# Kernel tuning notes

Measured on AMD Instinct MI355X. Metric: run time of the kernel, lower is better.

Reference implementation:

```python
import jax, jax.numpy as jnp
import numpy as np

SCALE = 0.0078125  # dequant scale from init_kwargs


def setup_inputs() -> dict:
    key = jax.random.key(0)
    k1, k2, k3 = jax.random.split(key, 3)
    B, S, D_IN, D_OUT = 4, 2048, 2048, 8192
    x = jax.random.normal(k1, (B, S, D_IN), dtype=jnp.float32)
    weight = jax.random.normal(k2, (D_OUT, D_IN), dtype=jnp.float32)  # torch Linear layout
    bias = jax.random.normal(k3, (D_OUT,), dtype=jnp.float32)
    return {"x": x, "weight": weight, "bias": bias}


def reference(x, weight, bias):
    # MATMUL.apply(x, weight.t(), bias, scale): scaled matmul + fused bias
    # out[b,s,o] = scale * sum_i x[b,s,i] * weight[o,i] + bias[o]
    out = jnp.einsum('bsi,oi->bso', x, weight) * jnp.asarray(SCALE, x.dtype)
    return out + bias
```

## Files before the change

### kernel.cpp

```cpp
#include <hip/hip_runtime.h>
#include <hip/hip_bf16.h>
#include <stdint.h>

typedef __bf16 bf16x8 __attribute__((ext_vector_type(8)));
typedef float  f32x4  __attribute__((ext_vector_type(4)));

static constexpr float kScale = 0.0078125f;

static __device__ __forceinline__ uint32_t bf16_rne(float f) {
  uint32_t u = __builtin_bit_cast(uint32_t, f);
  u += 0x7FFFu + ((u >> 16) & 1u);
  return u >> 16;
}
static __device__ __forceinline__ uint32_t pack2(float lo, float hi) {
  return bf16_rne(lo) | (bf16_rne(hi) << 16);
}

__global__ __launch_bounds__(256) void cvt_f32_to_bf16(
    const float* __restrict__ src, uint4* __restrict__ dst) {
  const int i = blockIdx.x * 256 + threadIdx.x;
  const float4* sv = reinterpret_cast<const float4*>(src);
  float4 a = sv[2 * i];
  float4 b = sv[2 * i + 1];
  uint4 o;
  o.x = pack2(a.x, a.y);
  o.y = pack2(a.z, a.w);
  o.z = pack2(b.x, b.y);
  o.w = pack2(b.z, b.w);
  dst[i] = o;
}

static __device__ __forceinline__ void gload_lds16(const void* g, void* l) {
  __builtin_amdgcn_global_load_lds(
      (const __attribute__((address_space(1))) void*)g,
      (__attribute__((address_space(3))) void*)l, 16, 0, 0);
}

#define BARRIER() __builtin_amdgcn_s_barrier()
#define LGKM0()                                        \
  do {                                                 \
    asm volatile("s_waitcnt lgkmcnt(0)" ::: "memory"); \
    __builtin_amdgcn_sched_barrier(0);                 \
  } while (0)
#define LGKM8() asm volatile("s_waitcnt lgkmcnt(8)" ::: "memory")
#define VMW(n)                                               \
  do {                                                       \
    asm volatile("s_waitcnt vmcnt(" #n ")" ::: "memory");    \
    __builtin_amdgcn_sched_barrier(0);                       \
  } while (0)

constexpr int TILE_V = (256 * 64) / 8;

template <int MH, int NH>
__device__ __forceinline__ void quad(f32x4 (&acc)[8][4],
                                     const bf16x8 (&aF)[4][2],
                                     const bf16x8 (&bF)[2][2]) {
  __builtin_amdgcn_s_setprio(1);
#pragma unroll
  for (int mi = 0; mi < 4; ++mi)
#pragma unroll
    for (int ni = 0; ni < 2; ++ni)
#pragma unroll
      for (int kk = 0; kk < 2; ++kk)
        acc[MH * 4 + mi][NH * 2 + ni] = __builtin_amdgcn_mfma_f32_16x16x32_bf16(
            aF[mi][kk], bF[ni][kk], acc[MH * 4 + mi][NH * 2 + ni], 0, 0, 0);
  __builtin_amdgcn_s_setprio(0);
}

template <int BUF, int MH>
__device__ __forceinline__ void loadA(bf16x8 (&aF)[4][2], const bf16x8* Av,
                                      int wr, int fr, int ac0) {
#pragma unroll
  for (int mi = 0; mi < 4; ++mi) {
    const int row = (MH << 7) + (wr << 6) + (mi << 4) + fr;
    aF[mi][0] = Av[BUF * TILE_V + row * 8 + ac0];
    aF[mi][1] = Av[BUF * TILE_V + row * 8 + (ac0 ^ 4)];
  }
}
template <int BUF, int NH>
__device__ __forceinline__ void loadB(bf16x8 (&bF)[2][2], const bf16x8* Bv,
                                      int wc, int fr, int ac0) {
#pragma unroll
  for (int ni = 0; ni < 2; ++ni) {
    const int row = (NH << 7) + (wc << 5) + (ni << 4) + fr;
    bF[ni][0] = Bv[BUF * TILE_V + row * 8 + ac0];
    bF[ni][1] = Bv[BUF * TILE_V + row * 8 + (ac0 ^ 4)];
  }
}

__global__ __launch_bounds__(512, 2) void gemm256_8phase(
    const uint16_t* __restrict__ A, const uint16_t* __restrict__ B,
    const float* __restrict__ bias, float* __restrict__ C,
    int Mi, int Ni, int Ki) {
  __shared__ __align__(16) uint16_t As[2][256 * 64];
  __shared__ __align__(16) uint16_t Bs[2][256 * 64];

  const int tid = threadIdx.x;
  const int l   = tid & 63;
  const int wv  = tid >> 6;
  const int wr  = wv >> 2;
  const int wc  = wv & 3;
  const int fr  = l & 15;
  const int fh  = l >> 4;
  const int l8  = l >> 3;
  const int l7  = l & 7;

  const int nbm = Mi >> 8, nbn = Ni >> 8;
  const int nwg = nbm * nbn;
  const int q = nwg >> 3, r = nwg & 7;
  const int xcd = (int)blockIdx.x & 7, orig = (int)blockIdx.x >> 3;
  const int swz = (xcd < r ? xcd * (q + 1) : r * (q + 1) + (xcd - r) * q) + orig;

  int bm, bn;
  if ((nbm & 7) == 0 && (nbn & 3) == 0) {
    const int s = swz >> 5;
    const int o = swz & 31;
    const int nsc = nbn >> 2;
    bm = (s / nsc) * 8 + (o >> 2);
    bn = (s % nsc) * 4 + (o & 3);
  } else {
    bm = swz / nbn;
    bn = swz % nbn;
  }

  const int xcol = (l7 ^ l8) << 3;
  const uint16_t* gA0 = A + (size_t)((bm << 8) + (wv << 3) + l8) * Ki + xcol;
  const uint16_t* gB0 = B + (size_t)((bn << 8) + (wv << 3) + l8) * Ki + xcol;

#define STAGE_A(bufi, chunk, t)                        \
  gload_lds16(gA0 + (size_t)(chunk) * Ki + (t) * 64,   \
              &As[bufi][((chunk) + (wv << 3)) << 6])
#define STAGE_B(bufi, chunk, t)                        \
  gload_lds16(gB0 + (size_t)(chunk) * Ki + (t) * 64,   \
              &Bs[bufi][((chunk) + (wv << 3)) << 6])

  const int ac0 = fh ^ (fr & 7);
  const bf16x8* Av = reinterpret_cast<const bf16x8*>(&As[0][0]);
  const bf16x8* Bv = reinterpret_cast<const bf16x8*>(&Bs[0][0]);

  f32x4 acc[8][4] = {};
  bf16x8 aF[4][2], b0[2][2], b1[2][2];

  const int NT = Ki >> 6;
  const int NI = NT >> 1;

  STAGE_A(0, 0, 0);   STAGE_A(0, 64, 0);
  STAGE_B(0, 0, 0);   STAGE_B(0, 64, 0);
  STAGE_B(0, 128, 0); STAGE_B(0, 192, 0);
  STAGE_A(0, 128, 0); STAGE_A(0, 192, 0);
  STAGE_A(1, 0, 1);   STAGE_A(1, 64, 1);
  STAGE_B(1, 0, 1);   STAGE_B(1, 64, 1);
  STAGE_B(1, 128, 1); STAGE_B(1, 192, 1);
  VMW(6);
  BARRIER();

#pragma unroll 1
  for (int i = 0; i < NI - 1; ++i) {
    const int t1 = 2 * i + 1, t2 = 2 * i + 2, t3 = 2 * i + 3;

    loadA<0, 0>(aF, Av, wr, fr, ac0);
    loadB<0, 0>(b0, Bv, wc, fr, ac0);
    STAGE_A(1, 128, t1); STAGE_A(1, 192, t1);
    LGKM8();
    BARRIER(); LGKM0();
    quad<0, 0>(acc, aF, b0);
    BARRIER();

    loadB<0, 1>(b1, Bv, wc, fr, ac0);
    STAGE_A(0, 0, t2); STAGE_A(0, 64, t2);
    BARRIER(); LGKM0();
    quad<0, 1>(acc, aF, b1);
    BARRIER();

    loadA<0, 1>(aF, Av, wr, fr, ac0);
    STAGE_B(0, 0, t2); STAGE_B(0, 64, t2);
    BARRIER(); LGKM0();
    quad<1, 0>(acc, aF, b0);
    BARRIER();

    STAGE_B(0, 128, t2); STAGE_B(0, 192, t2);
    VMW(6);
    BARRIER();
    quad<1, 1>(acc, aF, b1);
    BARRIER();

    loadA<1, 0>(aF, Av, wr, fr, ac0);
    loadB<1, 0>(b0, Bv, wc, fr, ac0);
    STAGE_A(0, 128, t2); STAGE_A(0, 192, t2);
    LGKM8();
    BARRIER(); LGKM0();
    quad<0, 0>(acc, aF, b0);
    BARRIER();

    loadB<1, 1>(b1, Bv, wc, fr, ac0);
    STAGE_A(1, 0, t3); STAGE_A(1, 64, t3);
    BARRIER(); LGKM0();
    quad<0, 1>(acc, aF, b1);
    BARRIER();

    loadA<1, 1>(aF, Av, wr, fr, ac0);
    STAGE_B(1, 0, t3); STAGE_B(1, 64, t3);
    BARRIER(); LGKM0();
    quad<1, 0>(acc, aF, b0);
    BARRIER();

    STAGE_B(1, 128, t3); STAGE_B(1, 192, t3);
    VMW(6);
    BARRIER();
    quad<1, 1>(acc, aF, b1);
    BARRIER();
  }

  {
    const int t1 = NT - 1;
    loadA<0, 0>(aF, Av, wr, fr, ac0);
    loadB<0, 0>(b0, Bv, wc, fr, ac0);
    STAGE_A(1, 128, t1); STAGE_A(1, 192, t1);
    LGKM8();
    BARRIER(); LGKM0();
    quad<0, 0>(acc, aF, b0);
    BARRIER();
    loadB<0, 1>(b1, Bv, wc, fr, ac0);
    BARRIER(); LGKM0();
    quad<0, 1>(acc, aF, b1);
    BARRIER();
    loadA<0, 1>(aF, Av, wr, fr, ac0);
    BARRIER(); LGKM0();
    quad<1, 0>(acc, aF, b0);
    BARRIER();
    VMW(0);
    BARRIER();
    quad<1, 1>(acc, aF, b1);
    BARRIER();
    loadA<1, 0>(aF, Av, wr, fr, ac0);
    loadB<1, 0>(b0, Bv, wc, fr, ac0);
    BARRIER(); LGKM0();
    quad<0, 0>(acc, aF, b0);
    BARRIER();
    loadB<1, 1>(b1, Bv, wc, fr, ac0);
    BARRIER(); LGKM0();
    quad<0, 1>(acc, aF, b1);
    BARRIER();
    loadA<1, 1>(aF, Av, wr, fr, ac0);
    BARRIER(); LGKM0();
    quad<1, 0>(acc, aF, b0);
    BARRIER();
    quad<1, 1>(acc, aF, b1);
  }

  const int rowB = (bm << 8) + (wr << 6);
  const int colB = (bn << 8) + (wc << 5);
#pragma unroll
  for (int n = 0; n < 4; ++n) {
    const int col = colB + (n >> 1) * 128 + (n & 1) * 16 + fr;
    const float bv = bias[col];
#pragma unroll
    for (int m = 0; m < 8; ++m) {
      const int row = rowB + (m >> 2) * 128 + (m & 3) * 16 + fh * 4;
#pragma unroll
      for (int j = 0; j < 4; ++j)
        C[(size_t)(row + j) * Ni + col] = acc[m][n][j] * kScale + bv;
    }
  }
}

__global__ __launch_bounds__(256) void gemm_bf16_bias(
    const uint16_t* __restrict__ A, const uint16_t* __restrict__ B,
    const float* __restrict__ bias, float* __restrict__ C,
    int Mi, int Ni, int Ki) {
  __shared__ __align__(16) uint16_t As[128 * 32];
  __shared__ __align__(16) uint16_t Bs[128 * 32];

  const int tid  = threadIdx.x;
  const int lane = tid & 63;
  const int wv   = tid >> 6;
  const int wr   = wv >> 1;
  const int wc   = wv & 1;
  const int fr   = lane & 15;
  const int fh   = lane >> 4;

  const int nTilesN = Ni >> 7;
  const int nwg = gridDim.x;
  const int q = nwg >> 3, r = nwg & 7;
  const int xcd = (int)blockIdx.x & 7, orig = (int)blockIdx.x >> 3;
  const int swz = (xcd < r ? xcd * (q + 1) : r * (q + 1) + (xcd - r) * q) + orig;
  const int bm = swz / nTilesN;
  const int bn = swz % nTilesN;

  const int sRow = tid >> 2;
  const int sCol = (tid & 3) << 3;

  const uint16_t* gA0 = A + (size_t)(bm * 128 + sRow) * Ki + sCol;
  const uint16_t* gA1 = gA0 + (size_t)64 * Ki;
  const uint16_t* gB0 = B + (size_t)(bn * 128 + sRow) * Ki + sCol;
  const uint16_t* gB1 = gB0 + (size_t)64 * Ki;
  uint16_t* lA0 = &As[tid * 8];
  uint16_t* lA1 = &As[(256 + tid) * 8];
  uint16_t* lB0 = &Bs[tid * 8];
  uint16_t* lB1 = &Bs[(256 + tid) * 8];

  const bf16x8* Av = reinterpret_cast<const bf16x8*>(As);
  const bf16x8* Bv = reinterpret_cast<const bf16x8*>(Bs);

  f32x4 acc[4][4] = {};

  for (int k0 = 0; k0 < Ki; k0 += 32) {
    gload_lds16(gA0 + k0, lA0);
    gload_lds16(gA1 + k0, lA1);
    gload_lds16(gB0 + k0, lB0);
    gload_lds16(gB1 + k0, lB1);
    __syncthreads();

    bf16x8 af[4], bfr[4];
#pragma unroll
    for (int m = 0; m < 4; ++m) af[m] = Av[(wr * 64 + m * 16 + fr) * 4 + fh];
#pragma unroll
    for (int n = 0; n < 4; ++n) bfr[n] = Bv[(wc * 64 + n * 16 + fr) * 4 + fh];

#pragma unroll
    for (int m = 0; m < 4; ++m)
#pragma unroll
      for (int n = 0; n < 4; ++n)
        acc[m][n] = __builtin_amdgcn_mfma_f32_16x16x32_bf16(af[m], bfr[n],
                                                            acc[m][n], 0, 0, 0);
    __syncthreads();
  }

  const int rowBase = bm * 128 + wr * 64;
  const int colBase = bn * 128 + wc * 64;
#pragma unroll
  for (int n = 0; n < 4; ++n) {
    const int col = colBase + n * 16 + fr;
    const float bv = bias[col];
#pragma unroll
    for (int m = 0; m < 4; ++m) {
      const int row = rowBase + m * 16 + fh * 4;
#pragma unroll
      for (int j = 0; j < 4; ++j)
        C[(size_t)(row + j) * Ni + col] = acc[m][n][j] * kScale + bv;
    }
  }
}

__global__ void naive_gemm(const float* __restrict__ x, const float* __restrict__ w,
                           const float* __restrict__ bias, float* __restrict__ out,
                           int Mi, int Ni, int Ki) {
  long idx = (long)blockIdx.x * blockDim.x + threadIdx.x;
  if (idx >= (long)Mi * Ni) return;
  int m = (int)(idx / Ni), n = (int)(idx % Ni);
  float s = 0.f;
  for (int k = 0; k < Ki; ++k) s += x[(long)m * Ki + k] * w[(long)n * Ki + k];
  out[idx] = s * kScale + bias[n];
}

extern "C" void kernel_launch(void* const* d_in, const int* in_sizes, int n_in,
                              void* d_out, int out_size, void* d_ws, size_t ws_size,
                              hipStream_t stream) {
  const float* x    = (const float*)d_in[0];
  const float* w    = (const float*)d_in[1];
  const float* bias = (const float*)d_in[2];
  float* out = (float*)d_out;

  const int Ni = in_sizes[2];
  const int Ki = in_sizes[1] / Ni;
  const int Mi = in_sizes[0] / Ki;

  const size_t nx = (size_t)Mi * Ki;
  const size_t nw = (size_t)Ni * Ki;

  if (ws_size >= (nx + nw) * sizeof(uint16_t) && (Ki % 32) == 0 &&
      (Mi % 128) == 0 && (Ni % 128) == 0) {
    uint16_t* xb = (uint16_t*)d_ws;
    uint16_t* wb = xb + nx;
    cvt_f32_to_bf16<<<(int)(nx / 2048), 256, 0, stream>>>(x, (uint4*)xb);
    cvt_f32_to_bf16<<<(int)(nw / 2048), 256, 0, stream>>>(w, (uint4*)wb);

    if ((Mi % 256) == 0 && (Ni % 256) == 0 && (Ki % 128) == 0 && Ki >= 256) {
      dim3 grid((Mi / 256) * (Ni / 256));
      gemm256_8phase<<<grid, 512, 0, stream>>>(xb, wb, bias, out, Mi, Ni, Ki);
    } else {
      dim3 grid((Mi / 128) * (Ni / 128));
      gemm_bf16_bias<<<grid, 256, 0, stream>>>(xb, wb, bias, out, Mi, Ni, Ki);
    }
  } else {
    long total = (long)Mi * Ni;
    naive_gemm<<<(int)((total + 255) / 256), 256, 0, stream>>>(x, w, bias, out,
                                                               Mi, Ni, Ki);
  }
}
```

Baseline: 379.9 us.

## Double-buffer A fragments and overlap LDS reads with MFMA quads

Adds a second A-fragment register set so that LDS-to-register loads for the next quad are issued before the current quad's MFMAs and overlap with them. The explicit lgkmcnt waits that serialized each fragment load before compute are removed, leaving waits to the compiler. Loads for the first quad of each iteration are hoisted into the previous iteration and the prologue. This costs extra VGPRs and depends on the compiler inserting correct waits, since the sched_barrier fences are gone.

```diff
diff --git a/kernel.cpp b/kernel.cpp
--- a/kernel.cpp
+++ b/kernel.cpp
@@ -37,12 +37,6 @@
 }
 
 #define BARRIER() __builtin_amdgcn_s_barrier()
-#define LGKM0()                                        \
-  do {                                                 \
-    asm volatile("s_waitcnt lgkmcnt(0)" ::: "memory"); \
-    __builtin_amdgcn_sched_barrier(0);                 \
-  } while (0)
-#define LGKM8() asm volatile("s_waitcnt lgkmcnt(8)" ::: "memory")
 #define VMW(n)                                               \
   do {                                                       \
     asm volatile("s_waitcnt vmcnt(" #n ")" ::: "memory");    \
@@ -139,7 +133,7 @@
   const bf16x8* Bv = reinterpret_cast<const bf16x8*>(&Bs[0][0]);
 
   f32x4 acc[8][4] = {};
-  bf16x8 aF[4][2], b0[2][2], b1[2][2];
+  bf16x8 aFX[4][2], aFY[4][2], b0[2][2], b1[2][2];
 
   const int NT = Ki >> 6;
   const int NI = NT >> 1;
@@ -153,99 +147,91 @@
   STAGE_B(1, 128, 1); STAGE_B(1, 192, 1);
   VMW(6);
   BARRIER();
+  loadA<0, 0>(aFX, Av, wr, fr, ac0);
+  loadB<0, 0>(b0, Bv, wc, fr, ac0);
 
 #pragma unroll 1
   for (int i = 0; i < NI - 1; ++i) {
     const int t1 = 2 * i + 1, t2 = 2 * i + 2, t3 = 2 * i + 3;
 
-    loadA<0, 0>(aF, Av, wr, fr, ac0);
-    loadB<0, 0>(b0, Bv, wc, fr, ac0);
     STAGE_A(1, 128, t1); STAGE_A(1, 192, t1);
-    LGKM8();
-    BARRIER(); LGKM0();
-    quad<0, 0>(acc, aF, b0);
-    BARRIER();
-
+    BARRIER();
     loadB<0, 1>(b1, Bv, wc, fr, ac0);
+    quad<0, 0>(acc, aFX, b0);
+    BARRIER();
+
     STAGE_A(0, 0, t2); STAGE_A(0, 64, t2);
-    BARRIER(); LGKM0();
-    quad<0, 1>(acc, aF, b1);
-    BARRIER();
-
-    loadA<0, 1>(aF, Av, wr, fr, ac0);
+    BARRIER();
+    loadA<0, 1>(aFY, Av, wr, fr, ac0);
+    quad<0, 1>(acc, aFX, b1);
+    BARRIER();
+
     STAGE_B(0, 0, t2); STAGE_B(0, 64, t2);
-    BARRIER(); LGKM0();
-    quad<1, 0>(acc, aF, b0);
+    BARRIER();
+    quad<1, 0>(acc, aFY, b0);
     BARRIER();
 
     STAGE_B(0, 128, t2); STAGE_B(0, 192, t2);
     VMW(6);
     BARRIER();
-    quad<1, 1>(acc, aF, b1);
-    BARRIER();
-
-    loadA<1, 0>(aF, Av, wr, fr, ac0);
+    loadA<1, 0>(aFX, Av, wr, fr, ac0);
     loadB<1, 0>(b0, Bv, wc, fr, ac0);
+    quad<1, 1>(acc, aFY, b1);
+    BARRIER();
+
     STAGE_A(0, 128, t2); STAGE_A(0, 192, t2);
-    LGKM8();
-    BARRIER(); LGKM0();
-    quad<0, 0>(acc, aF, b0);
-    BARRIER();
-
+    BARRIER();
     loadB<1, 1>(b1, Bv, wc, fr, ac0);
+    quad<0, 0>(acc, aFX, b0);
+    BARRIER();
+
     STAGE_A(1, 0, t3); STAGE_A(1, 64, t3);
-    BARRIER(); LGKM0();
-    quad<0, 1>(acc, aF, b1);
-    BARRIER();
-
-    loadA<1, 1>(aF, Av, wr, fr, ac0);
+    BARRIER();
+    loadA<1, 1>(aFY, Av, wr, fr, ac0);
+    quad<0, 1>(acc, aFX, b1);
+    BARRIER();
+
     STAGE_B(1, 0, t3); STAGE_B(1, 64, t3);
-    BARRIER(); LGKM0();
-    quad<1, 0>(acc, aF, b0);
+    BARRIER();
+    quad<1, 0>(acc, aFY, b0);
     BARRIER();
 
     STAGE_B(1, 128, t3); STAGE_B(1, 192, t3);
     VMW(6);
     BARRIER();
-    quad<1, 1>(acc, aF, b1);
+    loadA<0, 0>(aFX, Av, wr, fr, ac0);
+    loadB<0, 0>(b0, Bv, wc, fr, ac0);
+    quad<1, 1>(acc, aFY, b1);
     BARRIER();
   }
 
   {
-    const int t1 = NT - 1;
-    loadA<0, 0>(aF, Av, wr, fr, ac0);
-    loadB<0, 0>(b0, Bv, wc, fr, ac0);
-    STAGE_A(1, 128, t1); STAGE_A(1, 192, t1);
-    LGKM8();
-    BARRIER(); LGKM0();
-    quad<0, 0>(acc, aF, b0);
+    const int tL = NT - 1;
+    STAGE_A(1, 128, tL); STAGE_A(1, 192, tL);
     BARRIER();
     loadB<0, 1>(b1, Bv, wc, fr, ac0);
-    BARRIER(); LGKM0();
-    quad<0, 1>(acc, aF, b1);
-    BARRIER();
-    loadA<0, 1>(aF, Av, wr, fr, ac0);
-    BARRIER(); LGKM0();
-    quad<1, 0>(acc, aF, b0);
+    quad<0, 0>(acc, aFX, b0);
+    BARRIER();
+    loadA<0, 1>(aFY, Av, wr, fr, ac0);
+    quad<0, 1>(acc, aFX, b1);
+    BARRIER();
+    quad<1, 0>(acc, aFY, b0);
     BARRIER();
     VMW(0);
     BARRIER();
-    quad<1, 1>(acc, aF, b1);
-    BARRIER();
-    loadA<1, 0>(aF, Av, wr, fr, ac0);
+    loadA<1, 0>(aFX, Av, wr, fr, ac0);
     loadB<1, 0>(b0, Bv, wc, fr, ac0);
-    BARRIER(); LGKM0();
-    quad<0, 0>(acc, aF, b0);
+    quad<1, 1>(acc, aFY, b1);
     BARRIER();
     loadB<1, 1>(b1, Bv, wc, fr, ac0);
-    BARRIER(); LGKM0();
-    quad<0, 1>(acc, aF, b1);
-    BARRIER();
-    loadA<1, 1>(aF, Av, wr, fr, ac0);
-    BARRIER(); LGKM0();
-    quad<1, 0>(acc, aF, b0);
-    BARRIER();
-    quad<1, 1>(acc, aF, b1);
+    quad<0, 0>(acc, aFX, b0);
+    BARRIER();
+    loadA<1, 1>(aFY, Av, wr, fr, ac0);
+    quad<0, 1>(acc, aFX, b1);
+    BARRIER();
+    quad<1, 0>(acc, aFY, b0);
+    BARRIER();
+    quad<1, 1>(acc, aFY, b1);
   }
 
   const int rowB = (bm << 8) + (wr << 6);
```

Measured after the change: 856.9 us. +125.6%, slower.

## Switch GEMM inner MFMA from 16x16x32 to 32x32x16 bf16 tiles

Applied to the files above, without the earlier changes.

Replaces the per-wave 16x16x32 MFMA tiling with 32x32x16 MFMA instructions, reorganising fragment loads from LDS (four k-slices per 32-row fragment with the same XOR swizzle) and the accumulator layout and epilogue indexing. The larger MFMA shape cuts the number of instructions and LDS fragment reads per unit of work, which should raise matrix-core utilisation. It changes the register footprint and LDS access pattern, which could create bank conflicts or register pressure at 2 waves/SIMD occupancy.

```diff
diff --git a/kernel.cpp b/kernel.cpp
--- a/kernel.cpp
+++ b/kernel.cpp
@@ -4,6 +4,7 @@
 
 typedef __bf16 bf16x8 __attribute__((ext_vector_type(8)));
 typedef float  f32x4  __attribute__((ext_vector_type(4)));
+typedef float  f32x16 __attribute__((ext_vector_type(16)));
 
 static constexpr float kScale = 0.0078125f;
 
@@ -52,40 +53,37 @@
 constexpr int TILE_V = (256 * 64) / 8;
 
 template <int MH, int NH>
-__device__ __forceinline__ void quad(f32x4 (&acc)[8][4],
-                                     const bf16x8 (&aF)[4][2],
-                                     const bf16x8 (&bF)[2][2]) {
+__device__ __forceinline__ void quad32(f32x16 (&acc)[4][2],
+                                       const bf16x8 (&aF)[2][4],
+                                       const bf16x8 (&bF)[4]) {
   __builtin_amdgcn_s_setprio(1);
 #pragma unroll
-  for (int mi = 0; mi < 4; ++mi)
-#pragma unroll
-    for (int ni = 0; ni < 2; ++ni)
-#pragma unroll
-      for (int kk = 0; kk < 2; ++kk)
-        acc[MH * 4 + mi][NH * 2 + ni] = __builtin_amdgcn_mfma_f32_16x16x32_bf16(
-            aF[mi][kk], bF[ni][kk], acc[MH * 4 + mi][NH * 2 + ni], 0, 0, 0);
+  for (int ks = 0; ks < 4; ++ks)
+#pragma unroll
+    for (int mt = 0; mt < 2; ++mt)
+      acc[MH * 2 + mt][NH] = __builtin_amdgcn_mfma_f32_32x32x16_bf16(
+          aF[mt][ks], bF[ks], acc[MH * 2 + mt][NH], 0, 0, 0);
   __builtin_amdgcn_s_setprio(0);
 }
 
 template <int BUF, int MH>
-__device__ __forceinline__ void loadA(bf16x8 (&aF)[4][2], const bf16x8* Av,
-                                      int wr, int fr, int ac0) {
-#pragma unroll
-  for (int mi = 0; mi < 4; ++mi) {
-    const int row = (MH << 7) + (wr << 6) + (mi << 4) + fr;
-    aF[mi][0] = Av[BUF * TILE_V + row * 8 + ac0];
-    aF[mi][1] = Av[BUF * TILE_V + row * 8 + (ac0 ^ 4)];
+__device__ __forceinline__ void loadA32(bf16x8 (&aF)[2][4], const bf16x8* Av,
+                                        int wr, int l31, int lk, int l7) {
+#pragma unroll
+  for (int mt = 0; mt < 2; ++mt) {
+    const int row = (MH << 7) + (wr << 6) + (mt << 5) + l31;
+#pragma unroll
+    for (int ks = 0; ks < 4; ++ks)
+      aF[mt][ks] = Av[BUF * TILE_V + row * 8 + (((ks << 1) | lk) ^ l7)];
   }
 }
 template <int BUF, int NH>
-__device__ __forceinline__ void loadB(bf16x8 (&bF)[2][2], const bf16x8* Bv,
-                                      int wc, int fr, int ac0) {
-#pragma unroll
-  for (int ni = 0; ni < 2; ++ni) {
-    const int row = (NH << 7) + (wc << 5) + (ni << 4) + fr;
-    bF[ni][0] = Bv[BUF * TILE_V + row * 8 + ac0];
-    bF[ni][1] = Bv[BUF * TILE_V + row * 8 + (ac0 ^ 4)];
-  }
+__device__ __forceinline__ void loadB32(bf16x8 (&bF)[4], const bf16x8* Bv,
+                                        int wc, int l31, int lk, int l7) {
+  const int row = (NH << 7) + (wc << 5) + l31;
+#pragma unroll
+  for (int ks = 0; ks < 4; ++ks)
+    bF[ks] = Bv[BUF * TILE_V + row * 8 + (((ks << 1) | lk) ^ l7)];
 }
 
 __global__ __launch_bounds__(512, 2) void gemm256_8phase(
@@ -100,8 +98,8 @@
   const int wv  = tid >> 6;
   const int wr  = wv >> 2;
   const int wc  = wv & 3;
-  const int fr  = l & 15;
-  const int fh  = l >> 4;
+  const int l31 = l & 31;
+  const int lk  = l >> 5;
   const int l8  = l >> 3;
   const int l7  = l & 7;
 
@@ -134,12 +132,11 @@
   gload_lds16(gB0 + (size_t)(chunk) * Ki + (t) * 64,   \
               &Bs[bufi][((chunk) + (wv << 3)) << 6])
 
-  const int ac0 = fh ^ (fr & 7);
   const bf16x8* Av = reinterpret_cast<const bf16x8*>(&As[0][0]);
   const bf16x8* Bv = reinterpret_cast<const bf16x8*>(&Bs[0][0]);
 
-  f32x4 acc[8][4] = {};
-  bf16x8 aF[4][2], b0[2][2], b1[2][2];
+  f32x16 acc[4][2] = {};
+  bf16x8 aF[2][4], b0[4], b1[4];
 
   const int NT = Ki >> 6;
   const int NI = NT >> 1;
@@ -158,108 +155,110 @@
   for (int i = 0; i < NI - 1; ++i) {
     const int t1 = 2 * i + 1, t2 = 2 * i + 2, t3 = 2 * i + 3;
 
-    loadA<0, 0>(aF, Av, wr, fr, ac0);
-    loadB<0, 0>(b0, Bv, wc, fr, ac0);
+    loadA32<0, 0>(aF, Av, wr, l31, lk, l7);
+    loadB32<0, 0>(b0, Bv, wc, l31, lk, l7);
     STAGE_A(1, 128, t1); STAGE_A(1, 192, t1);
     LGKM8();
     BARRIER(); LGKM0();
-    quad<0, 0>(acc, aF, b0);
-    BARRIER();
-
-    loadB<0, 1>(b1, Bv, wc, fr, ac0);
+    quad32<0, 0>(acc, aF, b0);
+    BARRIER();
+
+    loadB32<0, 1>(b1, Bv, wc, l31, lk, l7);
     STAGE_A(0, 0, t2); STAGE_A(0, 64, t2);
     BARRIER(); LGKM0();
-    quad<0, 1>(acc, aF, b1);
-    BARRIER();
-
-    loadA<0, 1>(aF, Av, wr, fr, ac0);
+    quad32<0, 1>(acc, aF, b1);
+    BARRIER();
+
+    loadA32<0, 1>(aF, Av, wr, l31, lk, l7);
     STAGE_B(0, 0, t2); STAGE_B(0, 64, t2);
     BARRIER(); LGKM0();
-    quad<1, 0>(acc, aF, b0);
+    quad32<1, 0>(acc, aF, b0);
     BARRIER();
 
     STAGE_B(0, 128, t2); STAGE_B(0, 192, t2);
     VMW(6);
     BARRIER();
-    quad<1, 1>(acc, aF, b1);
-    BARRIER();
-
-    loadA<1, 0>(aF, Av, wr, fr, ac0);
-    loadB<1, 0>(b0, Bv, wc, fr, ac0);
+    quad32<1, 1>(acc, aF, b1);
+    BARRIER();
+
+    loadA32<1, 0>(aF, Av, wr, l31, lk, l7);
+    loadB32<1, 0>(b0, Bv, wc, l31, lk, l7);
     STAGE_A(0, 128, t2); STAGE_A(0, 192, t2);
     LGKM8();
     BARRIER(); LGKM0();
-    quad<0, 0>(acc, aF, b0);
-    BARRIER();
-
-    loadB<1, 1>(b1, Bv, wc, fr, ac0);
+    quad32<0, 0>(acc, aF, b0);
+    BARRIER();
+
+    loadB32<1, 1>(b1, Bv, wc, l31, lk, l7);
     STAGE_A(1, 0, t3); STAGE_A(1, 64, t3);
     BARRIER(); LGKM0();
-    quad<0, 1>(acc, aF, b1);
-    BARRIER();
-
-    loadA<1, 1>(aF, Av, wr, fr, ac0);
+    quad32<0, 1>(acc, aF, b1);
+    BARRIER();
+
+    loadA32<1, 1>(aF, Av, wr, l31, lk, l7);
     STAGE_B(1, 0, t3); STAGE_B(1, 64, t3);
     BARRIER(); LGKM0();
-    quad<1, 0>(acc, aF, b0);
+    quad32<1, 0>(acc, aF, b0);
     BARRIER();
 
     STAGE_B(1, 128, t3); STAGE_B(1, 192, t3);
     VMW(6);
     BARRIER();
-    quad<1, 1>(acc, aF, b1);
+    quad32<1, 1>(acc, aF, b1);
     BARRIER();
   }
 
   {
     const int t1 = NT - 1;
-    loadA<0, 0>(aF, Av, wr, fr, ac0);
-    loadB<0, 0>(b0, Bv, wc, fr, ac0);
+    loadA32<0, 0>(aF, Av, wr, l31, lk, l7);
+    loadB32<0, 0>(b0, Bv, wc, l31, lk, l7);
     STAGE_A(1, 128, t1); STAGE_A(1, 192, t1);
     LGKM8();
     BARRIER(); LGKM0();
-    quad<0, 0>(acc, aF, b0);
-    BARRIER();
-    loadB<0, 1>(b1, Bv, wc, fr, ac0);
-    BARRIER(); LGKM0();
-    quad<0, 1>(acc, aF, b1);
-    BARRIER();
-    loadA<0, 1>(aF, Av, wr, fr, ac0);
-    BARRIER(); LGKM0();
-    quad<1, 0>(acc, aF, b0);
+    quad32<0, 0>(acc, aF, b0);
+    BARRIER();
+    loadB32<0, 1>(b1, Bv, wc, l31, lk, l7);
+    BARRIER(); LGKM0();
+    quad32<0, 1>(acc, aF, b1);
+    BARRIER();
+    loadA32<0, 1>(aF, Av, wr, l31, lk, l7);
+    BARRIER(); LGKM0();
+    quad32<1, 0>(acc, aF, b0);
     BARRIER();
     VMW(0);
     BARRIER();
-    quad<1, 1>(acc, aF, b1);
-    BARRIER();
-    loadA<1, 0>(aF, Av, wr, fr, ac0);
-    loadB<1, 0>(b0, Bv, wc, fr, ac0);
-    BARRIER(); LGKM0();
-    quad<0, 0>(acc, aF, b0);
-    BARRIER();
-    loadB<1, 1>(b1, Bv, wc, fr, ac0);
-    BARRIER(); LGKM0();
-    quad<0, 1>(acc, aF, b1);
-    BARRIER();
-    loadA<1, 1>(aF, Av, wr, fr, ac0);
-    BARRIER(); LGKM0();
-    quad<1, 0>(acc, aF, b0);
-    BARRIER();
-    quad<1, 1>(acc, aF, b1);
-  }
-
-  const int rowB = (bm << 8) + (wr << 6);
-  const int colB = (bn << 8) + (wc << 5);
-#pragma unroll
-  for (int n = 0; n < 4; ++n) {
-    const int col = colB + (n >> 1) * 128 + (n & 1) * 16 + fr;
-    const float bv = bias[col];
-#pragma unroll
-    for (int m = 0; m < 8; ++m) {
-      const int row = rowB + (m >> 2) * 128 + (m & 3) * 16 + fh * 4;
-#pragma unroll
-      for (int j = 0; j < 4; ++j)
-        C[(size_t)(row + j) * Ni + col] = acc[m][n][j] * kScale + bv;
+    quad32<1, 1>(acc, aF, b1);
+    BARRIER();
+    loadA32<1, 0>(aF, Av, wr, l31, lk, l7);
+    loadB32<1, 0>(b0, Bv, wc, l31, lk, l7);
+    BARRIER(); LGKM0();
+    quad32<0, 0>(acc, aF, b0);
+    BARRIER();
+    loadB32<1, 1>(b1, Bv, wc, l31, lk, l7);
+    BARRIER(); LGKM0();
+    quad32<0, 1>(acc, aF, b1);
+    BARRIER();
+    loadA32<1, 1>(aF, Av, wr, l31, lk, l7);
+    BARRIER(); LGKM0();
+    quad32<1, 0>(acc, aF, b0);
+    BARRIER();
+    quad32<1, 1>(acc, aF, b1);
+  }
+
+  const int rowB = (bm << 8) + (wr << 6) + 4 * lk;
+  const int colB = (bn << 8) + (wc << 5) + l31;
+#pragma unroll
+  for (int mt4 = 0; mt4 < 4; ++mt4) {
+    const int rBase = rowB + (mt4 >> 1) * 128 + (mt4 & 1) * 32;
+#pragma unroll
+    for (int nh = 0; nh < 2; ++nh) {
+      const int col = colB + nh * 128;
+      const float bv = bias[col];
+#pragma unroll
+      for (int reg = 0; reg < 16; ++reg) {
+        const int row = rBase + (reg & 3) + 8 * (reg >> 2);
+        C[(size_t)row * Ni + col] = acc[mt4][nh][reg] * kScale + bv;
+      }
     }
   }
 }
```

After: 334.7 us. 1.13x faster.
